# Performance work log

Measured on AMD Instinct MI355X. Metric: run time of the kernel, lower is better.

Reference implementation:

```python
import jax, jax.numpy as jnp
import numpy as np
from jax import lax

B, L, D, H = 32, 512, 1024, 1024


def setup_inputs() -> dict:
    key = jax.random.key(0)
    kx, kw, kb = jax.random.split(key, 3)
    x = jax.random.normal(kx, (B, L, D), dtype=jnp.float32)
    # nn.Linear(D+H, 4H): weight (4H, D+H), bias (4H,), uniform(-1/sqrt(fan_in), 1/sqrt(fan_in))
    bound = 1.0 / np.sqrt(D + H)
    W = jax.random.uniform(kw, (4 * H, D + H), minval=-bound, maxval=bound, dtype=jnp.float32)
    b = jax.random.uniform(kb, (4 * H,), minval=-bound, maxval=bound, dtype=jnp.float32)
    return {"x": x, "W": W, "b": b}


def reference(x, W, b):
    Bsz, Lseq, Din = x.shape
    Hd = W.shape[0] // 4

    def step(carry, x_t):
        h, c = carry
        combined = jnp.concatenate([h, x_t], axis=-1)          # (B, H+D)
        gates = combined @ W.T + b                              # (B, 4H)
        f, i, o, c_tilde = jnp.split(gates, 4, axis=-1)
        c_new = jax.nn.sigmoid(f) * c + jax.nn.sigmoid(i) * jnp.tanh(c_tilde)
        h_new = jax.nn.sigmoid(o) * jnp.tanh(c_new)
        return (h_new, c_new), h_new

    h0 = jnp.zeros((Bsz, Hd), dtype=x.dtype)
    c0 = jnp.zeros((Bsz, Hd), dtype=x.dtype)
    xs = jnp.transpose(x, (1, 0, 2))                            # (L, B, D)
    _, hs = lax.scan(step, (h0, c0), xs)                        # hs: (L, B, H)
    return jnp.transpose(hs, (1, 0, 2))                         # (B, L, H)
```

## Files before the change

kernel.cpp:

```cpp
#include <hip/hip_runtime.h>
#include <hip/hip_fp16.h>

#define B_SZ 32
#define L_SZ 512
#define D_SZ 1024
#define H_SZ 1024
#define NG   4096
#define M_SZ 16384

typedef __attribute__((ext_vector_type(8))) short short8;
typedef __attribute__((ext_vector_type(4))) float f32x4;
typedef __attribute__((ext_vector_type(4))) unsigned u32x4;
typedef __attribute__((ext_vector_type(4))) unsigned short u16x4;

static const size_t GX_OFF  = 0;
static const size_t XB_OFF  = 134217728;
static const size_t WH_OFF  = 167772160;
static const size_t WX_OFF  = 176160768;
static const size_t FLG_OFF = 184680448;

__device__ __forceinline__ unsigned short f2bf(float f) {
  union { float f; unsigned u; } v; v.f = f;
  unsigned r = v.u + 0x7fffu + ((v.u >> 16) & 1u);
  return (unsigned short)(r >> 16);
}

__device__ __forceinline__ float fsig(float x) { return 1.f / (1.f + __expf(-x)); }
__device__ __forceinline__ float ftanh(float x) {
  x = fminf(fmaxf(x, -15.f), 15.f);
  float e = __expf(-2.f * x);
  return (1.f - e) / (1.f + e);
}

__device__ __forceinline__ void gload_lds16(const void* g, void* l) {
  __builtin_amdgcn_global_load_lds(
      (const __attribute__((address_space(1))) unsigned*)g,
      (__attribute__((address_space(3))) unsigned*)l, 16, 0, 0);
}


__global__ __launch_bounds__(256) void k_convert_w(const float* __restrict__ W,
                                                   unsigned short* __restrict__ Wh,
                                                   unsigned short* __restrict__ Wx) {
  int idx = blockIdx.x * 256 + threadIdx.x;
  f32x4 v = ((const f32x4*)W)[idx];
  u16x4 o;
#pragma unroll
  for (int e = 0; e < 4; ++e) o[e] = f2bf(v[e]);
  int n   = idx >> 9;
  int col = (idx & 511) * 4;
  if (col < 1024) *(u16x4*)(Wh + (size_t)n * 1024 + col)          = o;
  else            *(u16x4*)(Wx + (size_t)n * 1024 + (col - 1024)) = o;
}

__global__ __launch_bounds__(256) void k_convert_x(const float* __restrict__ x,
                                                   unsigned short* __restrict__ xb) {
  int idx = blockIdx.x * 256 + threadIdx.x;
  f32x4 v = ((const f32x4*)x)[idx];
  u16x4 o;
#pragma unroll
  for (int e = 0; e < 4; ++e) o[e] = f2bf(v[e]);
  unsigned long long val;
  __builtin_memcpy(&val, &o, 8);
  unsigned short* p = xb + (size_t)idx * 4;
  asm volatile("global_store_dwordx2 %0, %1, off sc0 sc1"
               :: "v"(p), "v"(val) : "memory");
}

__global__ __launch_bounds__(256) void k_zero_wt(unsigned* __restrict__ p, int n) {
  int i = blockIdx.x * 256 + threadIdx.x;
  unsigned z = 0u;
  if (i < n)
    asm volatile("global_store_dword %0, %1, off sc0 sc1"
                 :: "v"(p + i), "v"(z) : "memory");
}


__global__ __launch_bounds__(256) void k_xgemm(const unsigned short* __restrict__ A,
                                               const unsigned short* __restrict__ Bw,
                                               __half* __restrict__ C) {
  __shared__ unsigned short sA[128 * 64];
  __shared__ unsigned short sB[128 * 64];
  const int m0 = blockIdx.x * 128;
  const int n0 = blockIdx.y * 128;
  const int tid = threadIdx.x;
  const int lane = tid & 63;
  const int w = tid >> 6;
  const int wm = w >> 1, wn = w & 1;
  f32x4 acc[4][4] = {};
  for (int k0 = 0; k0 < 1024; k0 += 64) {
#pragma unroll
    for (int it = 0; it < 4; ++it) {
      int chunk = it * 256 + w * 64 + lane;
      int row = chunk >> 3, kc = chunk & 7;
      gload_lds16(A + (size_t)(m0 + row) * 1024 + k0 + kc * 8,
                  (char*)sA + (size_t)(it * 256 + w * 64) * 16);
      gload_lds16(Bw + (size_t)(n0 + row) * 1024 + k0 + kc * 8,
                  (char*)sB + (size_t)(it * 256 + w * 64) * 16);
    }
    asm volatile("s_waitcnt vmcnt(0)" ::: "memory");
    __syncthreads();
#pragma unroll
    for (int ks = 0; ks < 2; ++ks) {
      short8 af[4], bfr[4];
#pragma unroll
      for (int i = 0; i < 4; ++i) {
        int arow = wm * 64 + i * 16 + (lane & 15);
        af[i] = *(const short8*)(sA + arow * 64 + ks * 32 + (lane >> 4) * 8);
      }
#pragma unroll
      for (int j = 0; j < 4; ++j) {
        int brow = wn * 64 + j * 16 + (lane & 15);
        bfr[j] = *(const short8*)(sB + brow * 64 + ks * 32 + (lane >> 4) * 8);
      }
#pragma unroll
      for (int i = 0; i < 4; ++i)
#pragma unroll
        for (int j = 0; j < 4; ++j)
          acc[i][j] = __builtin_amdgcn_mfma_f32_16x16x32_bf16(af[i], bfr[j], acc[i][j], 0, 0, 0);
    }
    __syncthreads();
  }
#pragma unroll
  for (int i = 0; i < 4; ++i)
#pragma unroll
    for (int j = 0; j < 4; ++j)
#pragma unroll
      for (int q = 0; q < 4; ++q) {
        int row = m0 + wm * 64 + i * 16 + (lane >> 4) * 4 + q;
        int col = n0 + wn * 64 + j * 16 + (lane & 15);
        C[(size_t)row * NG + col] = __float2half(acc[i][j][q]);
      }
}


__global__ __launch_bounds__(256, 1) void k_lstm(const unsigned short* __restrict__ Whg,
                                                 const __half* __restrict__ Gx,
                                                 const float* __restrict__ bias,
                                                 unsigned short* __restrict__ ring,
                                                 float* __restrict__ out,
                                                 unsigned* __restrict__ flags) {
  extern __shared__ char lds[];
  char* h_base  = lds;
  float* part   = (float*)(lds + 65536);
  float* bias_s = (float*)(lds + 65536 + 18432);
  unsigned short* hlds = (unsigned short*)(lds + 65536 + 18432 + 128);

  const int tid = threadIdx.x;
  const int lane = tid & 63;
  const int wv = tid >> 6;
  const int wg = blockIdx.x;
  const int j0 = wg * 8;

  __builtin_amdgcn_fence(__ATOMIC_ACQUIRE, "agent");

  short8 bfrag[2][8];
#pragma unroll
  for (int ntx = 0; ntx < 2; ++ntx) {
#pragma unroll
    for (int ks = 0; ks < 8; ++ks) {
      int br = ntx * 16 + (lane & 15);
      const unsigned short* src = Whg
          + (size_t)((br >> 3) * 1024 + j0 + (br & 7)) * 1024
          + wv * 256 + ks * 32 + (lane >> 4) * 8;
      bfrag[ntx][ks] = *(const short8*)src;
    }
  }
  if (tid < 32) bias_s[tid] = bias[(tid >> 3) * 1024 + j0 + (tid & 7)];
  __syncthreads();

  const int row0 = lane & 15;
  const char* aB0 = h_base + row0 * 2048;
  const char* aB1 = h_base + (16 + row0) * 2048;
  const int kslot = (lane >> 4) * 16;
  const int aswz = (row0 & 7) << 4;
  const int kbyte0 = wv * 512;
  const int b_ = tid >> 3, jj = tid & 7;
  const float rb0 = bias_s[jj], rb1 = bias_s[8 + jj];
  const float rb2 = bias_s[16 + jj], rb3 = bias_s[24 + jj];
  float c_reg = 0.f;

  const unsigned* fp0 = flags + (size_t)(2 * tid) * 16;
  const unsigned* fp1 = flags + (size_t)(2 * tid + 1) * 16;

  for (int t = 0; t < 512; ++t) {
    const char* hin = (const char*)ring + (size_t)t * 65536;
    unsigned short* hout = ring + (size_t)(t + 1) * 32768;

    const char* gxp = (const char*)(Gx + ((size_t)(b_ * L_SZ + t)) * NG + j0 + jj);
    unsigned gxa, gxb, gxc, gxd;
    asm volatile("global_load_ushort %0, %1, off" : "=v"(gxa) : "v"(gxp)        : "memory");
    asm volatile("global_load_ushort %0, %1, off" : "=v"(gxb) : "v"(gxp + 2048) : "memory");
    asm volatile("global_load_ushort %0, %1, off" : "=v"(gxc) : "v"(gxp + 4096) : "memory");
    asm volatile("global_load_ushort %0, %1, off" : "=v"(gxd) : "v"(gxp + 6144) : "memory");

    if (t) {
#pragma unroll
      for (int it = 0; it < 16; ++it) {
        int i_ = it * 256 + tid;
        size_t src = ((size_t)i_ * 16) ^ (size_t)(((i_ >> 7) & 7) << 4);
        gload_lds16(hin + src,
                    h_base + (size_t)(it * 256 + (tid & 192)) * 16);
      }
    } else {
      u32x4 z = {0u, 0u, 0u, 0u};
#pragma unroll
      for (int it = 0; it < 16; ++it)
        *(u32x4*)(h_base + (size_t)(it * 256 + tid) * 16) = z;
    }
    asm volatile("s_waitcnt vmcnt(0)" ::: "memory");
    __builtin_amdgcn_sched_barrier(0);
    __syncthreads();

    f32x4 acc00 = {0.f,0.f,0.f,0.f}, acc01 = {0.f,0.f,0.f,0.f};
    f32x4 acc10 = {0.f,0.f,0.f,0.f}, acc11 = {0.f,0.f,0.f,0.f};
#pragma unroll
    for (int ks = 0; ks < 8; ++ks) {
      int kb = kbyte0 + ks * 64 + kslot;
      short8 a0 = *(const short8*)(aB0 + (kb ^ aswz));
      short8 a1 = *(const short8*)(aB1 + (kb ^ aswz));
      acc00 = __builtin_amdgcn_mfma_f32_16x16x32_bf16(a0, bfrag[0][ks], acc00, 0, 0, 0);
      acc01 = __builtin_amdgcn_mfma_f32_16x16x32_bf16(a0, bfrag[1][ks], acc01, 0, 0, 0);
      acc10 = __builtin_amdgcn_mfma_f32_16x16x32_bf16(a1, bfrag[0][ks], acc10, 0, 0, 0);
      acc11 = __builtin_amdgcn_mfma_f32_16x16x32_bf16(a1, bfrag[1][ks], acc11, 0, 0, 0);
    }
    {
      float* pw = part + wv * 1152;
      int r0 = (lane >> 4) * 4, cA = lane & 15;
#pragma unroll
      for (int q = 0; q < 4; ++q) {
        pw[(r0 + q) * 36 + cA]           = acc00[q];
        pw[(r0 + q) * 36 + 16 + cA]      = acc01[q];
        pw[(16 + r0 + q) * 36 + cA]      = acc10[q];
        pw[(16 + r0 + q) * 36 + 16 + cA] = acc11[q];
      }
    }
    __syncthreads();

    float s0 = 0.f, s1 = 0.f, s2 = 0.f, s3 = 0.f;
#pragma unroll
    for (int p = 0; p < 4; ++p) {
      const float* pp = part + p * 1152 + b_ * 36 + jj;
      s0 += pp[0]; s1 += pp[8]; s2 += pp[16]; s3 += pp[24];
    }
    float hn;
    {
      float sf = s0 + __half2float(__ushort_as_half((unsigned short)gxa)) + rb0;
      float si = s1 + __half2float(__ushort_as_half((unsigned short)gxb)) + rb1;
      float so = s2 + __half2float(__ushort_as_half((unsigned short)gxc)) + rb2;
      float sc = s3 + __half2float(__ushort_as_half((unsigned short)gxd)) + rb3;
      float cn = fsig(sf) * c_reg + fsig(si) * ftanh(sc);
      hn = fsig(so) * ftanh(cn);
      c_reg = cn;
      hlds[tid] = f2bf(hn);
    }
    float* outp = out + ((size_t)b_ * L_SZ + t) * H_SZ + j0 + jj;

    if (t < 511) {
      __syncthreads();
      if (tid < 32) {
        u32x4 v = *(u32x4*)(hlds + tid * 8);
        unsigned short* hp = hout + (size_t)tid * H_SZ + j0;
        asm volatile("global_store_dwordx4 %0, %1, off sc0 sc1"
                     :: "v"(hp), "v"(v) : "memory");
      }
      asm volatile("s_waitcnt vmcnt(0)" ::: "memory");
      if (tid == 0) {
        unsigned fv = (unsigned)(t + 1);
        const unsigned* myf = flags + (size_t)wg * 16;
        asm volatile("global_store_dword %0, %1, off sc0 sc1"
                     :: "v"(myf), "v"(fv) : "memory");
      }
      *outp = hn;
      if (tid < 64) {
        unsigned fa, fb;
        do {
          asm volatile("global_load_dword %0, %2, off sc0 sc1\n\t"
                       "global_load_dword %1, %3, off sc0 sc1\n\t"
                       "s_waitcnt vmcnt(0)"
                       : "=v"(fa), "=v"(fb) : "v"(fp0), "v"(fp1) : "memory");
        } while (!__all(fa > (unsigned)t && fb > (unsigned)t));
      }
      __syncthreads();
    } else {
      *outp = hn;
    }
  }
}


extern "C" void kernel_launch(void* const* d_in, const int* in_sizes, int n_in,
                              void* d_out, int out_size, void* d_ws, size_t ws_size,
                              hipStream_t stream) {
  const float* x = (const float*)d_in[0];
  const float* W = (const float*)d_in[1];
  const float* b = (const float*)d_in[2];
  char* ws = (char*)d_ws;
  __half* Gx           = (__half*)(ws + GX_OFF);
  unsigned short* xb   = (unsigned short*)(ws + XB_OFF);
  unsigned short* Wh   = (unsigned short*)(ws + WH_OFF);
  unsigned short* Wx   = (unsigned short*)(ws + WX_OFF);
  unsigned* flags      = (unsigned*)(ws + FLG_OFF);
  float* out = (float*)d_out;

  k_convert_w<<<8192, 256, 0, stream>>>(W, Wh, Wx);
  k_convert_x<<<16384, 256, 0, stream>>>(x, xb);
  k_zero_wt<<<8, 256, 0, stream>>>(flags, 8192 / 4);

  k_xgemm<<<dim3(128, 32), 256, 0, stream>>>(xb, Wx, Gx);

  (void)hipFuncSetAttribute((const void*)k_lstm,
                            hipFuncAttributeMaxDynamicSharedMemorySize, 84608);
  k_lstm<<<128, 256, 84608, stream>>>(Wh, Gx, b, xb, out, flags);
}
```

Before: 2.189 ms.

## Replace block-wide grid barrier with per-wave flag polling and K-sliced h loads

Each wave now polls only the 32 producer flags covering its own K-slice of h, then loads that slice into a private LDS region. This removes the block-wide __syncthreads between the h load and the MFMA loop. The flag publish moves to wave 1, so wave 0 no longer serialises the store, the flag and the poll. The aim is to shorten the critical path of the per-timestep grid synchronisation, so waves can start their partial GEMM as soon as their inputs are ready. The trade-off is finer-grained polling traffic and more complex correctness reasoning around the LDS reuse of part/hlds across steps.

```diff
diff --git a/kernel.cpp b/kernel.cpp
--- a/kernel.cpp
+++ b/kernel.cpp
@@ -141,10 +141,10 @@
                                                  float* __restrict__ out,
                                                  unsigned* __restrict__ flags) {
   extern __shared__ char lds[];
-  char* h_base  = lds;
+  char* h2      = lds;
   float* part   = (float*)(lds + 65536);
-  float* bias_s = (float*)(lds + 65536 + 18432);
-  unsigned short* hlds = (unsigned short*)(lds + 65536 + 18432 + 128);
+  float* bias_s = (float*)(lds + 83968);
+  unsigned short* hlds = (unsigned short*)(lds + 84096);
 
   const int tid = threadIdx.x;
   const int lane = tid & 63;
@@ -169,19 +169,15 @@
   if (tid < 32) bias_s[tid] = bias[(tid >> 3) * 1024 + j0 + (tid & 7)];
   __syncthreads();
 
-  const int row0 = lane & 15;
-  const char* aB0 = h_base + row0 * 2048;
-  const char* aB1 = h_base + (16 + row0) * 2048;
-  const int kslot = (lane >> 4) * 16;
-  const int aswz = (row0 & 7) << 4;
-  const int kbyte0 = wv * 512;
+  const int r0 = lane & 15;
+  char* aSlice = h2 + wv * 16384;
+  const int kcl = lane >> 4;
   const int b_ = tid >> 3, jj = tid & 7;
   const float rb0 = bias_s[jj], rb1 = bias_s[8 + jj];
   const float rb2 = bias_s[16 + jj], rb3 = bias_s[24 + jj];
   float c_reg = 0.f;
 
-  const unsigned* fp0 = flags + (size_t)(2 * tid) * 16;
-  const unsigned* fp1 = flags + (size_t)(2 * tid + 1) * 16;
+  const unsigned* myfp = flags + (size_t)(wv * 32 + (lane & 31)) * 16;
 
   for (int t = 0; t < 512; ++t) {
     const char* hin = (const char*)ring + (size_t)t * 65536;
@@ -195,30 +191,38 @@
     asm volatile("global_load_ushort %0, %1, off" : "=v"(gxd) : "v"(gxp + 6144) : "memory");
 
     if (t) {
-#pragma unroll
-      for (int it = 0; it < 16; ++it) {
-        int i_ = it * 256 + tid;
-        size_t src = ((size_t)i_ * 16) ^ (size_t)(((i_ >> 7) & 7) << 4);
-        gload_lds16(hin + src,
-                    h_base + (size_t)(it * 256 + (tid & 192)) * 16);
-      }
+      unsigned fa;
+      do {
+        asm volatile("global_load_dword %0, %1, off sc0 sc1\n\t"
+                     "s_waitcnt vmcnt(0)"
+                     : "=v"(fa) : "v"(myfp) : "memory");
+      } while (__any(fa < (unsigned)t));
+#pragma unroll
+      for (int j = 0; j < 16; ++j) {
+        int s = j * 64 + lane;
+        int row = s >> 5, kc = s & 31;
+        const char* src = hin + row * 2048 + wv * 512 + ((kc ^ (row & 7)) << 4);
+        gload_lds16(src, aSlice + j * 1024);
+      }
+      asm volatile("s_waitcnt vmcnt(0)" ::: "memory");
+      __builtin_amdgcn_sched_barrier(0);
     } else {
       u32x4 z = {0u, 0u, 0u, 0u};
 #pragma unroll
-      for (int it = 0; it < 16; ++it)
-        *(u32x4*)(h_base + (size_t)(it * 256 + tid) * 16) = z;
-    }
-    asm volatile("s_waitcnt vmcnt(0)" ::: "memory");
-    __builtin_amdgcn_sched_barrier(0);
-    __syncthreads();
+      for (int j = 0; j < 16; ++j)
+        *(u32x4*)(aSlice + j * 1024 + lane * 16) = z;
+      asm volatile("s_waitcnt vmcnt(0)" ::: "memory");
+      __builtin_amdgcn_sched_barrier(0);
+    }
 
     f32x4 acc00 = {0.f,0.f,0.f,0.f}, acc01 = {0.f,0.f,0.f,0.f};
     f32x4 acc10 = {0.f,0.f,0.f,0.f}, acc11 = {0.f,0.f,0.f,0.f};
 #pragma unroll
     for (int ks = 0; ks < 8; ++ks) {
-      int kb = kbyte0 + ks * 64 + kslot;
-      short8 a0 = *(const short8*)(aB0 + (kb ^ aswz));
-      short8 a1 = *(const short8*)(aB1 + (kb ^ aswz));
+      int kc = ks * 4 + kcl;
+      int off = (kc ^ (r0 & 7)) << 4;
+      short8 a0 = *(const short8*)(aSlice + r0 * 512 + off);
+      short8 a1 = *(const short8*)(aSlice + (16 + r0) * 512 + off);
       acc00 = __builtin_amdgcn_mfma_f32_16x16x32_bf16(a0, bfrag[0][ks], acc00, 0, 0, 0);
       acc01 = __builtin_amdgcn_mfma_f32_16x16x32_bf16(a0, bfrag[1][ks], acc01, 0, 0, 0);
       acc10 = __builtin_amdgcn_mfma_f32_16x16x32_bf16(a1, bfrag[0][ks], acc10, 0, 0, 0);
@@ -226,13 +230,13 @@
     }
     {
       float* pw = part + wv * 1152;
-      int r0 = (lane >> 4) * 4, cA = lane & 15;
+      int pr0 = (lane >> 4) * 4, cA = lane & 15;
 #pragma unroll
       for (int q = 0; q < 4; ++q) {
-        pw[(r0 + q) * 36 + cA]           = acc00[q];
-        pw[(r0 + q) * 36 + 16 + cA]      = acc01[q];
-        pw[(16 + r0 + q) * 36 + cA]      = acc10[q];
-        pw[(16 + r0 + q) * 36 + 16 + cA] = acc11[q];
+        pw[(pr0 + q) * 36 + cA]           = acc00[q];
+        pw[(pr0 + q) * 36 + 16 + cA]      = acc01[q];
+        pw[(16 + pr0 + q) * 36 + cA]      = acc10[q];
+        pw[(16 + pr0 + q) * 36 + 16 + cA] = acc11[q];
       }
     }
     __syncthreads();
@@ -254,36 +258,26 @@
       c_reg = cn;
       hlds[tid] = f2bf(hn);
     }
-    float* outp = out + ((size_t)b_ * L_SZ + t) * H_SZ + j0 + jj;
+    out[((size_t)b_ * L_SZ + t) * H_SZ + j0 + jj] = hn;
+    __syncthreads();
 
     if (t < 511) {
-      __syncthreads();
-      if (tid < 32) {
-        u32x4 v = *(u32x4*)(hlds + tid * 8);
-        unsigned short* hp = hout + (size_t)tid * H_SZ + j0;
+      if (tid >= 64 && tid < 96) {
+        int c = tid - 64;
+        u32x4 v = *(u32x4*)(hlds + c * 8);
+        unsigned short* hp = hout + (size_t)c * H_SZ + j0;
         asm volatile("global_store_dwordx4 %0, %1, off sc0 sc1"
                      :: "v"(hp), "v"(v) : "memory");
       }
-      asm volatile("s_waitcnt vmcnt(0)" ::: "memory");
-      if (tid == 0) {
-        unsigned fv = (unsigned)(t + 1);
-        const unsigned* myf = flags + (size_t)wg * 16;
-        asm volatile("global_store_dword %0, %1, off sc0 sc1"
-                     :: "v"(myf), "v"(fv) : "memory");
-      }
-      *outp = hn;
-      if (tid < 64) {
-        unsigned fa, fb;
-        do {
-          asm volatile("global_load_dword %0, %2, off sc0 sc1\n\t"
-                       "global_load_dword %1, %3, off sc0 sc1\n\t"
-                       "s_waitcnt vmcnt(0)"
-                       : "=v"(fa), "=v"(fb) : "v"(fp0), "v"(fp1) : "memory");
-        } while (!__all(fa > (unsigned)t && fb > (unsigned)t));
-      }
-      __syncthreads();
-    } else {
-      *outp = hn;
+      if (wv == 1) {
+        asm volatile("s_waitcnt vmcnt(0)" ::: "memory");
+        if (tid == 64) {
+          unsigned fv = (unsigned)(t + 1);
+          const unsigned* myf = flags + (size_t)wg * 16;
+          asm volatile("global_store_dword %0, %1, off sc0 sc1"
+                       :: "v"(myf), "v"(fv) : "memory");
+        }
+      }
     }
   }
 }
```

New measurement: 1.954 ms. 10.7% less time.
